# Performance work log

Measured on AMD Instinct MI355X. Metric: run time of the kernel, lower is better.

The kernel has to match this reference:

```python
import jax, jax.numpy as jnp
import numpy as np
import math

N_HEAD = 16
N_KV = 4


def setup_inputs() -> dict:
    key = jax.random.key(0)
    ks = jax.random.split(key, 10)
    B, T, C = 4, 2048, 1024
    hd = C // N_HEAD
    kv_dim = N_KV * hd  # 256
    s = 0.02
    return {
        "x": jax.random.normal(ks[0], (B, T, C), jnp.float32),
        "Wq": jax.random.normal(ks[1], (C, C), jnp.float32) * s,
        "bq": jax.random.normal(ks[2], (C,), jnp.float32) * s,
        "Wk": jax.random.normal(ks[3], (kv_dim, C), jnp.float32) * s,
        "bk": jax.random.normal(ks[4], (kv_dim,), jnp.float32) * s,
        "Wv": jax.random.normal(ks[5], (kv_dim, C), jnp.float32) * s,
        "bv": jax.random.normal(ks[6], (kv_dim,), jnp.float32) * s,
        "Wo": jax.random.normal(ks[7], (C, C), jnp.float32) * s,
        "bo": jax.random.normal(ks[8], (C,), jnp.float32) * s,
        "qk_gain": jnp.full((N_HEAD,), 5.5, jnp.float32),
    }


def reference(x, Wq, bq, Wk, bk, Wv, bv, Wo, bo, qk_gain):
    B, T, C = x.shape
    H, KV = N_HEAD, N_KV
    hd = C // H
    G = H // KV  # GQA group size

    # Projections (torch Linear: y = x @ W.T + b)
    q = (x @ Wq.T + bq).reshape(B, T, KV, G, hd).transpose(0, 2, 3, 1, 4)  # [B,KV,G,T,hd]
    k = (x @ Wk.T + bk).reshape(B, T, KV, hd).transpose(0, 2, 1, 3)        # [B,KV,T,hd]
    v = (x @ Wv.T + bv).reshape(B, T, KV, hd).transpose(0, 2, 1, 3)        # [B,KV,T,hd]

    # per-head gain on q; head order h = kv*G + g matches repeat_interleave
    q = q * qk_gain.reshape(1, KV, G, 1, 1)

    # GQA: contract each query group against its shared kv head (no KV replication)
    att = jnp.einsum('bkgtd,bksd->bkgts', q, k) / math.sqrt(hd)  # [B,KV,G,T,T]
    causal = jnp.tril(jnp.ones((T, T), bool))
    att = jnp.where(causal, att, -jnp.inf)
    att = jax.nn.softmax(att, axis=-1)

    y = jnp.einsum('bkgts,bksd->bkgtd', att, v)          # [B,KV,G,T,hd]
    y = y.transpose(0, 3, 1, 2, 4).reshape(B, T, C)      # [B,T,C]
    return y @ Wo.T + bo
```

## Files before the change

### kernel.cpp

```cpp
#include <hip/hip_runtime.h>
#include <hip/hip_bf16.h>

typedef __attribute__((ext_vector_type(8))) short bf16x8;
typedef __attribute__((ext_vector_type(4))) float f32x4;
typedef __attribute__((ext_vector_type(16))) float f32x16;
typedef __attribute__((ext_vector_type(2))) unsigned uint2v;

#define DEVI static __device__ __forceinline__

constexpr int Bb = 4, Tt = 2048, Cc = 1024, Hh = 16;
constexpr int Mrows = Bb * Tt;
constexpr int KVdim = 256;
constexpr float LOG2E = 1.44269504088896340736f;

DEVI unsigned short f2bf(float f) {
  union { float f; unsigned u; } v; v.f = f;
  unsigned r = v.u + 0x7fffu + ((v.u >> 16) & 1u);
  return (unsigned short)(r >> 16);
}

DEVI f32x4 mfma16(bf16x8 a, bf16x8 b, f32x4 c) {
  return __builtin_amdgcn_mfma_f32_16x16x32_bf16(a, b, c, 0, 0, 0);
}
DEVI f32x16 mfma32(bf16x8 a, bf16x8 b, f32x16 c) {
  return __builtin_amdgcn_mfma_f32_32x32x16_bf16(a, b, c, 0, 0, 0);
}

DEVI unsigned cvtpk(float lo, float hi) {
  unsigned w;
  asm("v_cvt_pk_bf16_f32 %0, %1, %2" : "=v"(w) : "v"(lo), "v"(hi));
  return w;
}

DEVI void load_lds16(const void* g, void* s) {
  __builtin_amdgcn_global_load_lds(
      (const __attribute__((address_space(1))) void*)g,
      (__attribute__((address_space(3))) void*)s, 16, 0, 0);
}

__global__ __launch_bounds__(256) void cvt_all(
    const float* __restrict__ s0, const float* __restrict__ s1,
    const float* __restrict__ s2, const float* __restrict__ s3,
    const float* __restrict__ s4,
    unsigned short* __restrict__ d0, unsigned short* __restrict__ d1,
    unsigned short* __restrict__ d2, unsigned short* __restrict__ d3,
    unsigned short* __restrict__ d4,
    int n0, int n1, int n2, int n3, int n4) {
  const float* s; unsigned short* d; int n;
  switch (blockIdx.y) {
    case 0: s = s0; d = d0; n = n0; break;
    case 1: s = s1; d = d1; n = n1; break;
    case 2: s = s2; d = d2; n = n2; break;
    case 3: s = s3; d = d3; n = n3; break;
    default: s = s4; d = d4; n = n4; break;
  }
  int i = (blockIdx.x * 256 + threadIdx.x) * 4;
  const int stride = gridDim.x * 256 * 4;
  for (; i < n; i += stride) {
    float4 v = *(const float4*)(s + i);
    ushort4 o;
    o.x = f2bf(v.x); o.y = f2bf(v.y); o.z = f2bf(v.z); o.w = f2bf(v.w);
    *(ushort4*)(d + i) = o;
  }
}

__global__ __launch_bounds__(256, 4) void qkv_gemm(const short* __restrict__ A,
                                                const short* __restrict__ wq,
                                                const short* __restrict__ wk,
                                                const short* __restrict__ wv,
                                                const float* __restrict__ bq,
                                                const float* __restrict__ bk,
                                                const float* __restrict__ bv,
                                                const float* __restrict__ gain,
                                                unsigned short* __restrict__ qout,
                                                unsigned short* __restrict__ kout,
                                                unsigned short* __restrict__ vout) {
  constexpr int K = Cc;
  __shared__ __align__(16) union QkvSmem {
    struct { short As[128 * 64]; short Bs[128 * 64]; } g;
    unsigned short Ls[64][136];
  } sm;
  short* As = sm.g.As;
  short* Bs = sm.g.Bs;
  const int tid = threadIdx.x;
  const int w = tid >> 6, l = tid & 63;
  const int l15 = l & 15, lg = l >> 4;
  const int m0 = blockIdx.x * 128, n0 = blockIdx.y * 128;

  const short* Bsrc; const float* bias; int mode;
  if (n0 < 1024)      { Bsrc = wq + (size_t)n0 * K;          bias = bq + n0;          mode = 0; }
  else if (n0 < 1280) { Bsrc = wk + (size_t)(n0 - 1024) * K; bias = bk + (n0 - 1024); mode = 1; }
  else                { Bsrc = wv + (size_t)(n0 - 1280) * K; bias = bv + (n0 - 1280); mode = 2; }

  const int wr = (w >> 1) * 64, wc = (w & 1) * 64;
  f32x4 acc[4][4] = {};

  const int lrow = l >> 3;
  const int lchk = (l & 7) ^ (lrow & 7);
  const short* gA = A + (size_t)(m0 + w * 32 + lrow) * K + lchk * 8;
  const short* gB = Bsrc + (size_t)(w * 32 + lrow) * K + lchk * 8;
  short* lA = As + w * 32 * 64;
  short* lB = Bs + w * 32 * 64;
  const int sw = l15 & 7;

  for (int k0 = 0; k0 < K; k0 += 64) {
#pragma unroll
    for (int i = 0; i < 4; ++i) {
      load_lds16(gA + (size_t)i * 8 * K, lA + i * 8 * 64);
      load_lds16(gB + (size_t)i * 8 * K, lB + i * 8 * 64);
    }
    gA += 64; gB += 64;
    __syncthreads();
    bf16x8 af[2][4], bfr[2][4];
#pragma unroll
    for (int kk = 0; kk < 2; ++kk)
#pragma unroll
      for (int i = 0; i < 4; ++i) {
        const int ch = ((kk * 4 + lg) ^ sw) << 3;
        af[kk][i] = *(const bf16x8*)(As + (wr + i * 16 + l15) * 64 + ch);
        bfr[kk][i] = *(const bf16x8*)(Bs + (wc + i * 16 + l15) * 64 + ch);
      }
#pragma unroll
    for (int kk = 0; kk < 2; ++kk)
#pragma unroll
      for (int mi = 0; mi < 4; ++mi)
#pragma unroll
        for (int ni = 0; ni < 4; ++ni)
          acc[mi][ni] = mfma16(af[kk][mi], bfr[kk][ni], acc[mi][ni]);
    __syncthreads();
  }

  const int crow = m0 + wr + lg * 4;
  if (mode == 2) {
    const int bb2 = m0 >> 11, tt0 = m0 & (Tt - 1);
#pragma unroll
    for (int colHalf = 0; colHalf < 2; ++colHalf) {
      if (colHalf) __syncthreads();
      if ((w & 1) == colHalf) {
#pragma unroll
        for (int ni = 0; ni < 4; ++ni) {
          const int c = ni * 16 + l15;
          const float bv_ = bias[colHalf * 64 + c];
#pragma unroll
          for (int mi = 0; mi < 4; ++mi)
#pragma unroll
            for (int r = 0; r < 4; ++r)
              sm.Ls[c][wr + lg * 4 + mi * 16 + r] = f2bf(acc[mi][ni][r] + bv_);
        }
      }
      __syncthreads();
      const int c = tid >> 2, ch = tid & 3;
      const int vcol = (n0 - 1280) + colHalf * 64 + c;
      unsigned short* dst = vout +
          ((size_t)((bb2 * 4 + (vcol >> 6)) * 64 + (vcol & 63))) * Tt + tt0 + ch * 32;
      const unsigned short* src = &sm.Ls[c][ch * 32];
#pragma unroll
      for (int q = 0; q < 4; ++q)
        *(bf16x8*)(dst + q * 8) = *(const bf16x8*)(src + q * 8);
    }
    return;
  }
#pragma unroll
  for (int ni = 0; ni < 4; ++ni) {
    const int lcol = wc + ni * 16 + l15;
    const float bv_ = bias[lcol];
    float sc = 1.f;
    if (mode == 0) sc = gain[(n0 + lcol) >> 6] * 0.125f * LOG2E;
#pragma unroll
    for (int mi = 0; mi < 4; ++mi) {
#pragma unroll
      for (int r = 0; r < 4; ++r) {
        const int row = crow + mi * 16 + r;
        float v = acc[mi][ni][r] + bv_;
        if (mode == 0) {
          qout[(size_t)row * Cc + n0 + lcol] = f2bf(v * sc);
        } else {
          kout[(size_t)row * KVdim + (n0 - 1024) + lcol] = f2bf(v);
        }
      }
    }
  }
}

__global__ __launch_bounds__(256, 4) void gemm_o(const short* __restrict__ A,
                                              const short* __restrict__ Bw,
                                              const float* __restrict__ bias,
                                              float* __restrict__ Cout,
                                              int M, int N, int K) {
  __shared__ __align__(16) short As[128 * 64];
  __shared__ __align__(16) short Bs[128 * 64];
  const int tid = threadIdx.x;
  const int w = tid >> 6, l = tid & 63;
  const int l15 = l & 15, lg = l >> 4;
  const int m0 = blockIdx.x * 128, n0 = blockIdx.y * 128;
  const int wr = (w >> 1) * 64, wc = (w & 1) * 64;
  f32x4 acc[4][4] = {};

  const int lrow = l >> 3;
  const int lchk = (l & 7) ^ (lrow & 7);
  const short* gA = A + (size_t)(m0 + w * 32 + lrow) * K + lchk * 8;
  const short* gB = Bw + (size_t)(n0 + w * 32 + lrow) * K + lchk * 8;
  short* lA = As + w * 32 * 64;
  short* lB = Bs + w * 32 * 64;
  const int sw = l15 & 7;

  for (int k0 = 0; k0 < K; k0 += 64) {
#pragma unroll
    for (int i = 0; i < 4; ++i) {
      load_lds16(gA + (size_t)i * 8 * K, lA + i * 8 * 64);
      load_lds16(gB + (size_t)i * 8 * K, lB + i * 8 * 64);
    }
    gA += 64; gB += 64;
    __syncthreads();
    bf16x8 af[2][4], bfr[2][4];
#pragma unroll
    for (int kk = 0; kk < 2; ++kk)
#pragma unroll
      for (int i = 0; i < 4; ++i) {
        const int ch = ((kk * 4 + lg) ^ sw) << 3;
        af[kk][i] = *(const bf16x8*)(As + (wr + i * 16 + l15) * 64 + ch);
        bfr[kk][i] = *(const bf16x8*)(Bs + (wc + i * 16 + l15) * 64 + ch);
      }
#pragma unroll
    for (int kk = 0; kk < 2; ++kk)
#pragma unroll
      for (int mi = 0; mi < 4; ++mi)
#pragma unroll
        for (int ni = 0; ni < 4; ++ni)
          acc[mi][ni] = mfma16(af[kk][mi], bfr[kk][ni], acc[mi][ni]);
    __syncthreads();
  }

  const int crow = m0 + wr + lg * 4;
  const int ccol = n0 + wc + l15;
#pragma unroll
  for (int ni = 0; ni < 4; ++ni) {
    const int col = ccol + ni * 16;
    const float bv = bias[col];
#pragma unroll
    for (int mi = 0; mi < 4; ++mi)
#pragma unroll
      for (int r = 0; r < 4; ++r)
        Cout[(size_t)(crow + mi * 16 + r) * N + col] = acc[mi][ni][r] + bv;
  }
}

#define PACK_SUB(pp, dst)                                        \
  {                                                              \
    unsigned Aw = cvtpk(pp[0], pp[1]), Bw_ = cvtpk(pp[2], pp[3]);\
    unsigned Cw = cvtpk(pp[4], pp[5]), Dw = cvtpk(pp[6], pp[7]); \
    uint2v xc = __builtin_amdgcn_permlane32_swap(Aw, Cw, false, false); \
    uint2v yd = __builtin_amdgcn_permlane32_swap(Bw_, Dw, false, false);\
    dst[0] = xc[0]; dst[1] = yd[0]; dst[2] = xc[1]; dst[3] = yd[1];     \
    Aw = cvtpk(pp[8], pp[9]); Bw_ = cvtpk(pp[10], pp[11]);       \
    Cw = cvtpk(pp[12], pp[13]); Dw = cvtpk(pp[14], pp[15]);      \
    xc = __builtin_amdgcn_permlane32_swap(Aw, Cw, false, false); \
    yd = __builtin_amdgcn_permlane32_swap(Bw_, Dw, false, false);\
    dst[4] = xc[0]; dst[5] = yd[0]; dst[6] = xc[1]; dst[7] = yd[1];     \
  }

#define HALF(ROFF, CB)                                                        \
  {                                                                           \
    f32x16 sa = {};                                                           \
    _Pragma("unroll")                                                         \
    for (int c = 0; c < 4; ++c) {                                             \
      bf16x8 ka = *(const bf16x8*)&Ks[kpar][(ROFF) + l31][c * 16 + hi * 8];   \
      sa = mfma32(ka, qf[c], sa);                                             \
    }                                                                         \
    if (s0 + (ROFF) + 31 > qw0) {                                             \
      _Pragma("unroll")                                                       \
      for (int r = 0; r < 16; ++r) {                                          \
        const int sl = s0 + (ROFF) + (r & 3) + 8 * (r >> 2) + 4 * hi;         \
        if (sl > q_abs) sa[r] = -1e30f;                                       \
      }                                                                       \
    }                                                                         \
    _Pragma("unroll")                                                         \
    for (int r = 0; r < 16; ++r) sa[r] = exp2f(sa[r]);                        \
    unsigned pw[8];                                                           \
    PACK_SUB(sa, pw);                                                         \
    _Pragma("unroll")                                                         \
    for (int t4 = 0; t4 < 2; ++t4) {                                          \
      union { unsigned u[4]; bf16x8 v; } pb;                                  \
      pb.u[0] = pw[t4 * 4 + 0]; pb.u[1] = pw[t4 * 4 + 1];                     \
      pb.u[2] = pw[t4 * 4 + 2]; pb.u[3] = pw[t4 * 4 + 3];                     \
      bf16x8 va0 = *(const bf16x8*)&Vt[kpar][l31][((CB) + t4) * 16 + hi * 8]; \
      bf16x8 va1 = *(const bf16x8*)&Vt[kpar][32 + l31][((CB) + t4) * 16 + hi * 8];\
      ot0 = mfma32(va0, pb.v, ot0);                                           \
      ot1 = mfma32(va1, pb.v, ot1);                                           \
      lacc = mfma32(onesf, pb.v, lacc);                                       \
    }                                                                         \
  }

__global__ __launch_bounds__(512, 4) void attn12(const short* __restrict__ qb,
                                                 const short* __restrict__ kb,
                                                 const short* __restrict__ vtg,
                                                 unsigned short* __restrict__ ob) {
  __shared__ __align__(16) union SmemU {
    struct { short Ks[2][64][72]; short Vt[2][64][72]; } s;
    struct { float red[256 * 32]; float redl[256]; } r;
  } sm;
  auto& Ks = sm.s.Ks;
  auto& Vt = sm.s.Vt;

  const int tid = threadIdx.x, w = tid >> 6, l = tid & 63;
  const int l31 = l & 31, hi = l >> 5;
  const int qsub = w & 3, kpar = w >> 2;
  const int id = blockIdx.x;
  const int bh = id & 63, j = id >> 6;
  const int i128 = 15 - j;
  const int b = bh >> 4, h = bh & 15, kv = h >> 2;
  const int q0 = i128 * 128;
  const int qw0 = q0 + qsub * 32;
  const int q_abs = qw0 + l31;

  const short* qp = qb + (size_t)(b * Tt + q_abs) * Cc + h * 64 + hi * 8;
  bf16x8 qf[4];
#pragma unroll
  for (int c = 0; c < 4; ++c) qf[c] = *(const bf16x8*)(qp + c * 16);

  bf16x8 onesf;
#pragma unroll
  for (int c = 0; c < 8; ++c) onesf[c] = (short)0x3F80;

  f32x16 ot0 = {}, ot1 = {}, lacc = {};

  const int half512 = tid >> 8;
  const int srow = (tid & 255) >> 2, scol = (tid & 3) * 16;
  const short* kst = kb + (size_t)(b * Tt + srow) * KVdim + kv * 64 + scol;
  const short* vst = vtg + (size_t)((b * 4 + kv) * 64 + srow) * Tt + scol;

  const int ntiles = 2 * i128 + 2;

  bf16x8 rk0, rk1, rv0, rv1;
  {
    const short* ks = kst + (size_t)half512 * 64 * KVdim;
    const short* vs = vst + half512 * 64;
    rk0 = *(const bf16x8*)ks;  rk1 = *(const bf16x8*)(ks + 8);
    rv0 = *(const bf16x8*)vs;  rv1 = *(const bf16x8*)(vs + 8);
  }

  for (int tp = 0; tp < ntiles; tp += 2) {
    *(bf16x8*)&Ks[half512][srow][scol] = rk0;
    *(bf16x8*)&Ks[half512][srow][scol + 8] = rk1;
    *(bf16x8*)&Vt[half512][srow][scol] = rv0;
    *(bf16x8*)&Vt[half512][srow][scol + 8] = rv1;
    __syncthreads();
    const int ts = tp + 2 + half512;
    if (ts < ntiles) {
      const short* ks = kst + (size_t)ts * 64 * KVdim;
      const short* vs = vst + ts * 64;
      rk0 = *(const bf16x8*)ks;  rk1 = *(const bf16x8*)(ks + 8);
      rv0 = *(const bf16x8*)vs;  rv1 = *(const bf16x8*)(vs + 8);
    }
    const int t = tp + kpar;
    if (t < ntiles) {
      const int s0 = t * 64;
      if (s0 <= qw0 + 31) {
        HALF(0, 0);
        if (s0 + 32 <= qw0 + 31) HALF(32, 2);
      }
    }
    __syncthreads();
  }

  const float l_w = lacc[0];

  float* red = sm.r.red;
  float* redl = sm.r.redl;
  const int rot = l & 7;
  if (kpar == 1) {
    float* p = red + ((qsub * 64 + l) * 32);
#pragma unroll
    for (int c = 0; c < 8; ++c) {
      const int cc = ((c + rot) & 7) * 4;
      f32x4 v;
      if (c < 4) {
        v[0] = ot0[c * 4]; v[1] = ot0[c * 4 + 1];
        v[2] = ot0[c * 4 + 2]; v[3] = ot0[c * 4 + 3];
      } else {
        const int b0 = (c - 4) * 4;
        v[0] = ot1[b0]; v[1] = ot1[b0 + 1];
        v[2] = ot1[b0 + 2]; v[3] = ot1[b0 + 3];
      }
      *(f32x4*)(p + cc) = v;
    }
    redl[qsub * 64 + l] = l_w;
  }
  __syncthreads();
  if (kpar == 0) {
    const float* p = red + ((qsub * 64 + l) * 32);
    f32x16 o0 = ot0, o1 = ot1;
#pragma unroll
    for (int c = 0; c < 8; ++c) {
      const int cc = ((c + rot) & 7) * 4;
      f32x4 v = *(const f32x4*)(p + cc);
      if (c < 4) {
        o0[c * 4] += v[0]; o0[c * 4 + 1] += v[1];
        o0[c * 4 + 2] += v[2]; o0[c * 4 + 3] += v[3];
      } else {
        const int b0 = (c - 4) * 4;
        o1[b0] += v[0]; o1[b0 + 1] += v[1];
        o1[b0 + 2] += v[2]; o1[b0 + 3] += v[3];
      }
    }
    const float l_s = l_w + redl[qsub * 64 + l];
    const float inv = 1.f / l_s;
    unsigned short* op = ob + (size_t)(b * Tt + q_abs) * Cc + h * 64;
#pragma unroll
    for (int r = 0; r < 16; ++r) {
      const int d = (r & 3) + 8 * (r >> 2) + 4 * hi;
      op[d] = f2bf(o0[r] * inv);
      op[32 + d] = f2bf(o1[r] * inv);
    }
  }
}

extern "C" void kernel_launch(void* const* d_in, const int* in_sizes, int n_in,
                              void* d_out, int out_size, void* d_ws, size_t ws_size,
                              hipStream_t stream) {
  (void)in_sizes; (void)n_in; (void)out_size; (void)ws_size;
  const float* x  = (const float*)d_in[0];
  const float* Wq = (const float*)d_in[1];
  const float* bq = (const float*)d_in[2];
  const float* Wk = (const float*)d_in[3];
  const float* bk = (const float*)d_in[4];
  const float* Wv = (const float*)d_in[5];
  const float* bv = (const float*)d_in[6];
  const float* Wo = (const float*)d_in[7];
  const float* bo = (const float*)d_in[8];
  const float* gain = (const float*)d_in[9];
  float* out = (float*)d_out;

  char* ws = (char*)d_ws;
  short* xb  = (short*)ws;                    ws += (size_t)Mrows * Cc * 2;
  short* qbf = (short*)ws;                    ws += (size_t)Mrows * Cc * 2;
  short* kbf = (short*)ws;                    ws += (size_t)Mrows * KVdim * 2;
  short* vtg = (short*)ws;                    ws += (size_t)Mrows * KVdim * 2;
  short* atb = (short*)ws;                    ws += (size_t)Mrows * Cc * 2;
  short* wqb = (short*)ws;                    ws += (size_t)Cc * Cc * 2;
  short* wkb = (short*)ws;                    ws += (size_t)KVdim * Cc * 2;
  short* wvb = (short*)ws;                    ws += (size_t)KVdim * Cc * 2;
  short* wob = (short*)ws;                    ws += (size_t)Cc * Cc * 2;

  cvt_all<<<dim3(1024, 5), 256, 0, stream>>>(
      x, Wq, Wk, Wv, Wo,
      (unsigned short*)xb, (unsigned short*)wqb, (unsigned short*)wkb,
      (unsigned short*)wvb, (unsigned short*)wob,
      Mrows * Cc, Cc * Cc, KVdim * Cc, KVdim * Cc, Cc * Cc);

  qkv_gemm<<<dim3(Mrows / 128, 12), 256, 0, stream>>>(
      xb, wqb, wkb, wvb, bq, bk, bv, gain,
      (unsigned short*)qbf, (unsigned short*)kbf, (unsigned short*)vtg);

  attn12<<<1024, 512, 0, stream>>>(qbf, kbf, vtg, (unsigned short*)atb);

  gemm_o<<<dim3(Mrows / 128, Cc / 128), 256, 0, stream>>>(
      atb, wob, bo, out, Mrows, Cc, Cc);
}
```

Measured before the change: 127.9 us.

## Double-buffer LDS tiles in QKV and output GEMMs with prefetched K-loop

```diff
diff --git a/kernel.cpp b/kernel.cpp
--- a/kernel.cpp
+++ b/kernel.cpp
@@ -64,7 +64,56 @@
   }
 }
 
-__global__ __launch_bounds__(256, 4) void qkv_gemm(const short* __restrict__ A,
+#define GEMM_COMPUTE(ASBUF, BSBUF)                                            \
+  {                                                                           \
+    bf16x8 af[2][4], bfr[2][4];                                               \
+    _Pragma("unroll")                                                         \
+    for (int kk = 0; kk < 2; ++kk)                                            \
+      _Pragma("unroll")                                                       \
+      for (int i = 0; i < 4; ++i) {                                           \
+        const int ch = ((kk * 4 + lg) ^ sw) << 3;                             \
+        af[kk][i] = *(const bf16x8*)((ASBUF) + (wr + i * 16 + l15) * 64 + ch);\
+        bfr[kk][i] = *(const bf16x8*)((BSBUF) + (wc + i * 16 + l15) * 64 + ch);\
+      }                                                                       \
+    _Pragma("unroll")                                                         \
+    for (int kk = 0; kk < 2; ++kk)                                            \
+      _Pragma("unroll")                                                       \
+      for (int mi = 0; mi < 4; ++mi)                                          \
+        _Pragma("unroll")                                                     \
+        for (int ni = 0; ni < 4; ++ni)                                        \
+          acc[mi][ni] = mfma16(af[kk][mi], bfr[kk][ni], acc[mi][ni]);         \
+  }
+
+#define GEMM_STAGE(buf)                                                       \
+  {                                                                           \
+    _Pragma("unroll")                                                         \
+    for (int i = 0; i < 4; ++i) {                                             \
+      load_lds16(gA + (size_t)i * 8 * 1024, lA + (buf) * 8192 + i * 8 * 64);  \
+      load_lds16(gB + (size_t)i * 8 * 1024, lB + (buf) * 8192 + i * 8 * 64);  \
+    }                                                                         \
+    gA += 64; gB += 64;                                                       \
+  }
+
+#define GEMM_KLOOP                                                            \
+  GEMM_STAGE(0);                                                              \
+  GEMM_STAGE(1);                                                              \
+  for (int kt = 0; kt < 15; ++kt) {                                           \
+    const int cur = kt & 1;                                                   \
+    asm volatile("s_waitcnt vmcnt(8)" ::: "memory");                          \
+    __builtin_amdgcn_s_barrier();                                             \
+    __builtin_amdgcn_sched_barrier(0);                                        \
+    GEMM_COMPUTE(As + cur * 8192, Bs + cur * 8192);                           \
+    __builtin_amdgcn_sched_barrier(0);                                        \
+    __builtin_amdgcn_s_barrier();                                             \
+    __builtin_amdgcn_sched_barrier(0);                                        \
+    if (kt < 14) GEMM_STAGE(cur);                                             \
+  }                                                                           \
+  asm volatile("s_waitcnt vmcnt(0)" ::: "memory");                            \
+  __builtin_amdgcn_s_barrier();                                               \
+  __builtin_amdgcn_sched_barrier(0);                                          \
+  GEMM_COMPUTE(As + 8192, Bs + 8192);
+
+__global__ __launch_bounds__(256, 2) void qkv_gemm(const short* __restrict__ A,
                                                 const short* __restrict__ wq,
                                                 const short* __restrict__ wk,
                                                 const short* __restrict__ wv,
@@ -77,11 +126,11 @@
                                                 unsigned short* __restrict__ vout) {
   constexpr int K = Cc;
   __shared__ __align__(16) union QkvSmem {
-    struct { short As[128 * 64]; short Bs[128 * 64]; } g;
+    struct { short As[2][128 * 64]; short Bs[2][128 * 64]; } g;
     unsigned short Ls[64][136];
   } sm;
-  short* As = sm.g.As;
-  short* Bs = sm.g.Bs;
+  short* As = &sm.g.As[0][0];
+  short* Bs = &sm.g.Bs[0][0];
   const int tid = threadIdx.x;
   const int w = tid >> 6, l = tid & 63;
   const int l15 = l & 15, lg = l >> 4;
@@ -103,35 +152,11 @@
   short* lB = Bs + w * 32 * 64;
   const int sw = l15 & 7;
 
-  for (int k0 = 0; k0 < K; k0 += 64) {
-#pragma unroll
-    for (int i = 0; i < 4; ++i) {
-      load_lds16(gA + (size_t)i * 8 * K, lA + i * 8 * 64);
-      load_lds16(gB + (size_t)i * 8 * K, lB + i * 8 * 64);
-    }
-    gA += 64; gB += 64;
-    __syncthreads();
-    bf16x8 af[2][4], bfr[2][4];
-#pragma unroll
-    for (int kk = 0; kk < 2; ++kk)
-#pragma unroll
-      for (int i = 0; i < 4; ++i) {
-        const int ch = ((kk * 4 + lg) ^ sw) << 3;
-        af[kk][i] = *(const bf16x8*)(As + (wr + i * 16 + l15) * 64 + ch);
-        bfr[kk][i] = *(const bf16x8*)(Bs + (wc + i * 16 + l15) * 64 + ch);
-      }
-#pragma unroll
-    for (int kk = 0; kk < 2; ++kk)
-#pragma unroll
-      for (int mi = 0; mi < 4; ++mi)
-#pragma unroll
-        for (int ni = 0; ni < 4; ++ni)
-          acc[mi][ni] = mfma16(af[kk][mi], bfr[kk][ni], acc[mi][ni]);
-    __syncthreads();
-  }
+  GEMM_KLOOP;
 
   const int crow = m0 + wr + lg * 4;
   if (mode == 2) {
+    __syncthreads();
     const int bb2 = m0 >> 11, tt0 = m0 & (Tt - 1);
 #pragma unroll
     for (int colHalf = 0; colHalf < 2; ++colHalf) {
@@ -182,13 +207,14 @@
   }
 }
 
-__global__ __launch_bounds__(256, 4) void gemm_o(const short* __restrict__ A,
+__global__ __launch_bounds__(256, 2) void gemm_o(const short* __restrict__ A,
                                               const short* __restrict__ Bw,
                                               const float* __restrict__ bias,
                                               float* __restrict__ Cout,
-                                              int M, int N, int K) {
-  __shared__ __align__(16) short As[128 * 64];
-  __shared__ __align__(16) short Bs[128 * 64];
+                                              int M, int N, int Kd) {
+  __shared__ __align__(16) short As[2][128 * 64];
+  __shared__ __align__(16) short Bs_[2][128 * 64];
+  short* Bs = &Bs_[0][0];
   const int tid = threadIdx.x;
   const int w = tid >> 6, l = tid & 63;
   const int l15 = l & 15, lg = l >> 4;
@@ -198,37 +224,33 @@
 
   const int lrow = l >> 3;
   const int lchk = (l & 7) ^ (lrow & 7);
-  const short* gA = A + (size_t)(m0 + w * 32 + lrow) * K + lchk * 8;
-  const short* gB = Bw + (size_t)(n0 + w * 32 + lrow) * K + lchk * 8;
-  short* lA = As + w * 32 * 64;
+  const short* gA = A + (size_t)(m0 + w * 32 + lrow) * 1024 + lchk * 8;
+  const short* gB = Bw + (size_t)(n0 + w * 32 + lrow) * 1024 + lchk * 8;
+  short* lA = &As[0][0] + w * 32 * 64;
   short* lB = Bs + w * 32 * 64;
   const int sw = l15 & 7;
 
-  for (int k0 = 0; k0 < K; k0 += 64) {
-#pragma unroll
-    for (int i = 0; i < 4; ++i) {
-      load_lds16(gA + (size_t)i * 8 * K, lA + i * 8 * 64);
-      load_lds16(gB + (size_t)i * 8 * K, lB + i * 8 * 64);
-    }
-    gA += 64; gB += 64;
-    __syncthreads();
-    bf16x8 af[2][4], bfr[2][4];
-#pragma unroll
-    for (int kk = 0; kk < 2; ++kk)
-#pragma unroll
-      for (int i = 0; i < 4; ++i) {
-        const int ch = ((kk * 4 + lg) ^ sw) << 3;
-        af[kk][i] = *(const bf16x8*)(As + (wr + i * 16 + l15) * 64 + ch);
-        bfr[kk][i] = *(const bf16x8*)(Bs + (wc + i * 16 + l15) * 64 + ch);
-      }
-#pragma unroll
-    for (int kk = 0; kk < 2; ++kk)
-#pragma unroll
-      for (int mi = 0; mi < 4; ++mi)
-#pragma unroll
-        for (int ni = 0; ni < 4; ++ni)
-          acc[mi][ni] = mfma16(af[kk][mi], bfr[kk][ni], acc[mi][ni]);
-    __syncthreads();
+  {
+    short* As2 = &As[0][0];
+#define AsX As2
+    GEMM_STAGE(0);
+    GEMM_STAGE(1);
+    for (int kt = 0; kt < 15; ++kt) {
+      const int cur = kt & 1;
+      asm volatile("s_waitcnt vmcnt(8)" ::: "memory");
+      __builtin_amdgcn_s_barrier();
+      __builtin_amdgcn_sched_barrier(0);
+      GEMM_COMPUTE(As2 + cur * 8192, Bs + cur * 8192);
+      __builtin_amdgcn_sched_barrier(0);
+      __builtin_amdgcn_s_barrier();
+      __builtin_amdgcn_sched_barrier(0);
+      if (kt < 14) GEMM_STAGE(cur);
+    }
+    asm volatile("s_waitcnt vmcnt(0)" ::: "memory");
+    __builtin_amdgcn_s_barrier();
+    __builtin_amdgcn_sched_barrier(0);
+    GEMM_COMPUTE(As2 + 8192, Bs + 8192);
+#undef AsX
   }
 
   const int crow = m0 + wr + lg * 4;
```

Result: no change. 128.3 us (+0.3%).
